# Optimization experiments

Measured on AMD Instinct MI355X. Metric: run time of the kernel, lower is better.

The kernel has to match this reference:

```python
import jax, jax.numpy as jnp
import numpy as np

CLIP_FRAMES = 16
CLIP_STRIDE = 8
D_CODE = 256
K_CODE = 8192
ENC_DIM = 128 * CLIP_FRAMES * 4 * 4  # 32768
EPS = 1e-5


def setup_inputs() -> dict:
    key = jax.random.key(0)
    ks = jax.random.split(key, 16)
    rn = lambda k, s, sc: (jax.random.normal(k, s, jnp.float32) * sc)
    inp = {}
    inp['x'] = jax.random.normal(ks[0], (4, 3, 64, 96, 96), jnp.float32)
    inp['conv1_w'] = rn(ks[1], (32, 3, 3, 3, 3), 0.1)
    inp['conv1_b'] = jnp.zeros((32,), jnp.float32)
    inp['bn1_g'] = jnp.ones((32,), jnp.float32)
    inp['bn1_b'] = jnp.zeros((32,), jnp.float32)
    inp['conv2_w'] = rn(ks[2], (64, 32, 3, 3, 3), 0.05)
    inp['conv2_b'] = jnp.zeros((64,), jnp.float32)
    inp['bn2_g'] = jnp.ones((64,), jnp.float32)
    inp['bn2_b'] = jnp.zeros((64,), jnp.float32)
    inp['conv3_w'] = rn(ks[3], (128, 64, 3, 3, 3), 0.04)
    inp['conv3_b'] = jnp.zeros((128,), jnp.float32)
    inp['bn3_g'] = jnp.ones((128,), jnp.float32)
    inp['bn3_b'] = jnp.zeros((128,), jnp.float32)
    inp['proj_w'] = rn(ks[4], (D_CODE, ENC_DIM), 0.005)
    inp['proj_b'] = jnp.zeros((D_CODE,), jnp.float32)
    inp['codebook'] = jax.random.uniform(ks[5], (K_CODE, D_CODE), jnp.float32, -1.0 / K_CODE, 1.0 / K_CODE)
    inp['gru_w_ih'] = rn(ks[6], (3 * D_CODE, D_CODE), 0.05)
    inp['gru_w_hh'] = rn(ks[7], (3 * D_CODE, D_CODE), 0.05)
    inp['gru_b_ih'] = jnp.zeros((3 * D_CODE,), jnp.float32)
    inp['gru_b_hh'] = jnp.zeros((3 * D_CODE,), jnp.float32)
    return inp


def _conv3d(x, w, b):
    y = jax.lax.conv_general_dilated(x, w, (1, 1, 1), ((1, 1), (1, 1), (1, 1)),
                                     dimension_numbers=('NCDHW', 'OIDHW', 'NCDHW'))
    return y + b[None, :, None, None, None]


def _bn(x, g, b):
    # training-mode BatchNorm3d: batch stats over (N,D,H,W), biased variance
    m = x.mean(axis=(0, 2, 3, 4), keepdims=True)
    v = ((x - m) ** 2).mean(axis=(0, 2, 3, 4), keepdims=True)
    return g[None, :, None, None, None] * (x - m) * jax.lax.rsqrt(v + EPS) + b[None, :, None, None, None]


def _maxpool(x):
    return jax.lax.reduce_window(x, -jnp.inf, jax.lax.max, (1, 1, 1, 2, 2), (1, 1, 1, 2, 2), 'VALID')


def _adaptive_avgpool(x):
    # [N,128,16,24,24] -> [N,128,16,4,4]; 24/4=6 exact window
    s = jax.lax.reduce_window(x, 0.0, jax.lax.add, (1, 1, 1, 6, 6), (1, 1, 1, 6, 6), 'VALID')
    return s / 36.0


def _gru(xs, w_ih, w_hh, b_ih, b_hh):
    # torch GRU, batch_first, h0=0. xs: [B,L,D]
    B, L, D = xs.shape
    gx = jnp.einsum('bld,gd->blg', xs, w_ih) + b_ih  # [B,L,3D]

    def step(h, gx_t):
        gh = h @ w_hh.T + b_hh
        xr, xz, xn = jnp.split(gx_t, 3, axis=-1)
        hr, hz, hn = jnp.split(gh, 3, axis=-1)
        r = jax.nn.sigmoid(xr + hr)
        z = jax.nn.sigmoid(xz + hz)
        n = jnp.tanh(xn + r * hn)
        h2 = (1.0 - z) * n + z * h
        return h2, h2

    h0 = jnp.zeros((B, D), xs.dtype)
    _, ys = jax.lax.scan(step, h0, jnp.swapaxes(gx, 0, 1))
    return jnp.swapaxes(ys, 0, 1)  # [B,L,D]


def _forward(x, conv1_w, conv1_b, bn1_g, bn1_b, conv2_w, conv2_b, bn2_g, bn2_b,
             conv3_w, conv3_b, bn3_g, bn3_b, proj_w, proj_b, codebook,
             gru_w_ih, gru_w_hh, gru_b_ih, gru_b_hh):
    B, C, T, H, W = x.shape
    num_clips = max(1, (T - CLIP_FRAMES) // CLIP_STRIDE + 1)
    clips = jnp.stack([x[:, :, i * CLIP_STRIDE:i * CLIP_STRIDE + CLIP_FRAMES] for i in range(num_clips)])

    def encode(clip):  # clip: [B,3,16,96,96]; BN stats per-clip like the torch loop
        h = jax.nn.relu(_bn(_conv3d(clip, conv1_w, conv1_b), bn1_g, bn1_b))
        h = _maxpool(h)
        h = jax.nn.relu(_bn(_conv3d(h, conv2_w, conv2_b), bn2_g, bn2_b))
        h = _maxpool(h)
        h = jax.nn.relu(_bn(_conv3d(h, conv3_w, conv3_b), bn3_g, bn3_b))
        h = _adaptive_avgpool(h)            # [B,128,16,4,4]
        h = h.reshape(B, -1)                # [B, 32768]
        return h @ proj_w.T + proj_b        # [B, D_CODE]

    features = jnp.swapaxes(jax.vmap(encode)(clips), 0, 1)  # [B,L,D]
    L, D = features.shape[1], features.shape[2]

    # quantize: squared-Euclidean argmin (same argmin as torch.cdist p=2)
    flat = features.reshape(-1, D)
    d2 = (flat * flat).sum(-1, keepdims=True) - 2.0 * flat @ codebook.T + (codebook * codebook).sum(-1)
    token_indices = jnp.argmin(d2, axis=-1)
    quantized = codebook[token_indices].reshape(B, L, D)

    sg = jax.lax.stop_gradient
    commitment_loss = jnp.mean((features - sg(quantized)) ** 2)
    codebook_loss = jnp.mean((quantized - sg(features)) ** 2)
    context_features = _gru(quantized[:, :-1], gru_w_ih, gru_w_hh, gru_b_ih, gru_b_hh)
    context_loss = jnp.mean((context_features - features[:, 1:]) ** 2)
    vq_loss = commitment_loss + 0.25 * codebook_loss + 0.1 * context_loss
    return token_indices.reshape(B, L), quantized, commitment_loss, codebook_loss, context_loss, vq_loss


def reference(x, conv1_w, conv1_b, bn1_g, bn1_b, conv2_w, conv2_b, bn2_g, bn2_b,
              conv3_w, conv3_b, bn3_g, bn3_b, proj_w, proj_b, codebook,
              gru_w_ih, gru_w_hh, gru_b_ih, gru_b_hh):
    return _forward(x, conv1_w, conv1_b, bn1_g, bn1_b, conv2_w, conv2_b, bn2_g, bn2_b,
                    conv3_w, conv3_b, bn3_g, bn3_b, proj_w, proj_b, codebook,
                    gru_w_ih, gru_w_hh, gru_b_ih, gru_b_hh)
```

## Files before the change

### kernel.cpp

```cpp
#include <hip/hip_runtime.h>
#include <math.h>


typedef __attribute__((ext_vector_type(8))) short short8;
typedef __attribute__((ext_vector_type(4))) float f32x4;

__device__ inline unsigned short f2bf(float x) {
    unsigned int u = __float_as_uint(x);
    u += 0x7FFFu + ((u >> 16) & 1u);
    return (unsigned short)(u >> 16);
}
__device__ inline float bf2f(unsigned short h) {
    return __uint_as_float(((unsigned int)h) << 16);
}
__device__ inline f32x4 vmax4(f32x4 a, f32x4 b) {
    return (f32x4){fmaxf(a.x, b.x), fmaxf(a.y, b.y), fmaxf(a.z, b.z), fmaxf(a.w, b.w)};
}
__device__ inline f32x4 vmin4(f32x4 a, f32x4 b) {
    return (f32x4){fminf(a.x, b.x), fminf(a.y, b.y), fminf(a.z, b.z), fminf(a.w, b.w)};
}

#define C1LOADR(J) \
    f32x4 u = *(const f32x4*)(ip + (J) * 36); \
    f32x4 w4 = *(const f32x4*)(ip + (J) * 36 + 4); \
    f32x4 sA = u; \
    f32x4 sB = __builtin_shufflevector(u, w4, 1, 2, 3, 4); \
    f32x4 sC = __builtin_shufflevector(u, w4, 2, 3, 4, 5);
#define C1UPD0(I) a0_##I += wa0 * sA + wa1 * sB + wa2 * sC; a1_##I += wb0 * sA + wb1 * sB + wb2 * sC;
#define C1UPD1(I) a0_##I += wa3 * sA + wa4 * sB + wa5 * sC; a1_##I += wb3 * sA + wb4 * sB + wb5 * sC;
#define C1UPD2(I) a0_##I += wa6 * sA + wa7 * sB + wa8 * sC; a1_##I += wb6 * sA + wb7 * sB + wb8 * sC;

__launch_bounds__(256, 3)
__global__ void conv1k(const float* __restrict__ x, const float* __restrict__ wgt,
                       const float* __restrict__ bias, float* __restrict__ pmax,
                       float* __restrict__ pmin, float* __restrict__ stats, int t0) {
    int bb = blockIdx.x;
    int xt = bb % 3; int yt = (bb / 3) % 4; int t = (bb / 12) % 16; int n = bb / 192;
    int x0 = xt * 32, y0 = yt * 24;
    __shared__ float tile[9 * 936];
    __shared__ float wl[3456];
    __shared__ float sst[64];
    int tid = threadIdx.x;
    for (int i = tid; i < 3456; i += 256) {
        int idx = i % 12; int r = i / 12;
        int co = r & 31; int p = r >> 5;
        wl[i] = idx < 9 ? wgt[co * 81 + p * 9 + idx] : 0.f;
    }
    if (tid < 64) sst[tid] = 0.f;
    for (int i = tid; i < 7956; i += 256) {
        int p = i / 884; int rem = i % 884;
        int r = rem / 34, cl = rem % 34;
        int ci = p / 3, kt = p % 3;
        int lt = t + kt - 1;
        int yy = y0 + r - 1, xx = x0 + cl - 1;
        float v = 0.f;
        if (lt >= 0 && lt <= 15 && yy >= 0 && yy < 96 && xx >= 0 && xx < 96)
            v = x[((size_t)(n * 3 + ci) * 64 + (t0 + lt)) * 9216 + yy * 96 + cl + x0 - 1];
        tile[p * 936 + r * 36 + cl] = v;
    }
    __syncthreads();

    int cg = tid & 15;
    int co0 = cg * 2;
    float bv0 = bias[co0], bv1 = bias[co0 + 1];
    float ls0 = 0.f, lq0 = 0.f, ls1 = 0.f, lq1 = 0.f;
    size_t nt48 = (size_t)(n * 16 + t) * 48;

    #pragma unroll 1
    for (int rr = 0; rr < 3; ++rr) {
        int sp = rr * 16 + (tid >> 4);
        int tx = sp & 7, ty = sp >> 3;
        f32x4 a0_0 = (f32x4)bv0, a0_1 = (f32x4)bv0, a0_2 = (f32x4)bv0, a0_3 = (f32x4)bv0;
        f32x4 a1_0 = (f32x4)bv1, a1_1 = (f32x4)bv1, a1_2 = (f32x4)bv1, a1_3 = (f32x4)bv1;

        #pragma unroll 1
        for (int p = 0; p < 9; ++p) {
            const float* wpk = wl + ((p * 32 + co0) * 12);
            f32x4 wv0 = *(const f32x4*)(wpk);
            f32x4 wv1 = *(const f32x4*)(wpk + 4);
            f32x4 wv2 = *(const f32x4*)(wpk + 8);
            f32x4 wv3 = *(const f32x4*)(wpk + 12);
            f32x4 wv4 = *(const f32x4*)(wpk + 16);
            f32x4 wv5 = *(const f32x4*)(wpk + 20);
            float wa0 = wv0.x, wa1 = wv0.y, wa2 = wv0.z, wa3 = wv0.w;
            float wa4 = wv1.x, wa5 = wv1.y, wa6 = wv1.z, wa7 = wv1.w;
            float wa8 = wv2.x;
            float wb0 = wv3.x, wb1 = wv3.y, wb2 = wv3.z, wb3 = wv3.w;
            float wb4 = wv4.x, wb5 = wv4.y, wb6 = wv4.z, wb7 = wv4.w;
            float wb8 = wv5.x;
            const float* ip = tile + p * 936 + (ty * 4) * 36 + tx * 4;
            { C1LOADR(0) C1UPD0(0) }
            { C1LOADR(1) C1UPD0(1) C1UPD1(0) }
            { C1LOADR(2) C1UPD0(2) C1UPD1(1) C1UPD2(0) }
            { C1LOADR(3) C1UPD0(3) C1UPD1(2) C1UPD2(1) }
            { C1LOADR(4) C1UPD1(3) C1UPD2(2) }
            { C1LOADR(5) C1UPD2(3) }
        }

        f32x4 s4 = a0_0 + a0_1 + a0_2 + a0_3;
        ls0 += s4.x + s4.y + s4.z + s4.w;
        f32x4 q4 = a0_0 * a0_0 + a0_1 * a0_1 + a0_2 * a0_2 + a0_3 * a0_3;
        lq0 += q4.x + q4.y + q4.z + q4.w;
        f32x4 s5 = a1_0 + a1_1 + a1_2 + a1_3;
        ls1 += s5.x + s5.y + s5.z + s5.w;
        f32x4 q5 = a1_0 * a1_0 + a1_1 * a1_1 + a1_2 * a1_2 + a1_3 * a1_3;
        lq1 += q5.x + q5.y + q5.z + q5.w;

        f32x4 mx0a = vmax4(a0_0, a0_1), mx0b = vmax4(a0_2, a0_3);
        f32x4 mn0a = vmin4(a0_0, a0_1), mn0b = vmin4(a0_2, a0_3);
        f32x4 mx1a = vmax4(a1_0, a1_1), mx1b = vmax4(a1_2, a1_3);
        f32x4 mn1a = vmin4(a1_0, a1_1), mn1b = vmin4(a1_2, a1_3);
        size_t row0 = (nt48 + (size_t)(yt * 12 + ty * 2)) * 1536 + (size_t)(xt * 16 + tx * 2) * 32 + co0;
        size_t row1 = row0 + 1536;
        *(float2*)(pmax + row0)      = make_float2(fmaxf(mx0a.x, mx0a.y), fmaxf(mx1a.x, mx1a.y));
        *(float2*)(pmax + row0 + 32) = make_float2(fmaxf(mx0a.z, mx0a.w), fmaxf(mx1a.z, mx1a.w));
        *(float2*)(pmax + row1)      = make_float2(fmaxf(mx0b.x, mx0b.y), fmaxf(mx1b.x, mx1b.y));
        *(float2*)(pmax + row1 + 32) = make_float2(fmaxf(mx0b.z, mx0b.w), fmaxf(mx1b.z, mx1b.w));
        *(float2*)(pmin + row0)      = make_float2(fminf(mn0a.x, mn0a.y), fminf(mn1a.x, mn1a.y));
        *(float2*)(pmin + row0 + 32) = make_float2(fminf(mn0a.z, mn0a.w), fminf(mn1a.z, mn1a.w));
        *(float2*)(pmin + row1)      = make_float2(fminf(mn0b.x, mn0b.y), fminf(mn1b.x, mn1b.y));
        *(float2*)(pmin + row1 + 32) = make_float2(fminf(mn0b.z, mn0b.w), fminf(mn1b.z, mn1b.w));
    }

    ls0 += __shfl_xor(ls0, 16, 64); ls0 += __shfl_xor(ls0, 32, 64);
    lq0 += __shfl_xor(lq0, 16, 64); lq0 += __shfl_xor(lq0, 32, 64);
    ls1 += __shfl_xor(ls1, 16, 64); ls1 += __shfl_xor(ls1, 32, 64);
    lq1 += __shfl_xor(lq1, 16, 64); lq1 += __shfl_xor(lq1, 32, 64);
    if ((tid & 63) < 16) {
        atomicAdd(&sst[co0 * 2], ls0);
        atomicAdd(&sst[co0 * 2 + 1], lq0);
        atomicAdd(&sst[co0 * 2 + 2], ls1);
        atomicAdd(&sst[co0 * 2 + 3], lq1);
    }
    __syncthreads();
    if (tid < 64) atomicAdd(&stats[tid], sst[tid]);
}

__global__ void bnpool1b(const float* __restrict__ pmax, const float* __restrict__ pmin,
                         const float* __restrict__ st, const float* __restrict__ gam,
                         const float* __restrict__ bet,
                         unsigned short* __restrict__ phi, unsigned short* __restrict__ plo) {
    int i = blockIdx.x * 256 + threadIdx.x;
    int c8 = i & 3; int xo = (i >> 2) % 48; int yo = (i / 192) % 48;
    int t = (i / 9216) % 16; int n = i / 147456;
    size_t base = (((size_t)(n * 16 + t) * 48 + yo) * 48 + xo) * 32 + c8 * 8;
    union { unsigned short s[8]; uint4 v; } Uh, Ul;
    #pragma unroll
    for (int j = 0; j < 8; ++j) {
        int ch = c8 * 8 + j;
        float mean = st[ch * 2] * (1.f / 589824.f);
        float var  = st[ch * 2 + 1] * (1.f / 589824.f) - mean * mean;
        var = var < 0.f ? 0.f : var;
        float sc = gam[ch] / sqrtf(var + 1e-5f);
        float sh = bet[ch] - mean * sc;
        float pv = sc >= 0.f ? pmax[base + j] : pmin[base + j];
        float v = fmaxf(sc * pv + sh, 0.f);
        Uh.s[j] = f2bf(v);
        Ul.s[j] = f2bf(v - bf2f(Uh.s[j]));
    }
    size_t off = ((((size_t)n * 18 + t + 1) * 50 + yo + 1) * 52 + (xo + 1)) * 32 + c8 * 8;
    *(uint4*)(phi + off) = Uh.v;
    *(uint4*)(plo + off) = Ul.v;
}

__launch_bounds__(256, 2)
__global__ void conv2k(const unsigned short* __restrict__ phi, const unsigned short* __restrict__ plo,
                       const unsigned short* __restrict__ w2p, const float* __restrict__ bias,
                       float* __restrict__ out, float* __restrict__ st) {
    __shared__ unsigned short lds[36864];
    __shared__ float sred[4][64], qred[4][64];
    int b = blockIdx.x;
    int y0 = (b % 12) * 4; int t = (b / 12) % 16; int n = b / 192;
    int wv = threadIdx.x >> 6, lane = threadIdx.x & 63;
    int c = lane & 15, q = lane >> 4;
    int y = y0 + wv;

    f32x4 acc[4][3];
    #pragma unroll
    for (int i = 0; i < 4; ++i)
        #pragma unroll
        for (int j = 0; j < 3; ++j) acc[i][j] = (f32x4)0.f;

    const int laneoff = c * 32 + q * 8;
    for (int kt = 0; kt < 3; ++kt) {
        const uint4* src = (const uint4*)(w2p + kt * 36864);
        uint4* dst = (uint4*)lds;
        __syncthreads();
        for (int i = threadIdx.x; i < 4608; i += 256) dst[i] = src[i];
        __syncthreads();
        const unsigned short* ph_t = phi + ((size_t)(n * 18 + t + kt) * 50) * (52 * 32);
        const unsigned short* pl_t = plo + ((size_t)(n * 18 + t + kt) * 50) * (52 * 32);
        #pragma unroll
        for (int ky = 0; ky < 3; ++ky) {
            const unsigned short* rowh = ph_t + (y + ky) * (52 * 32) + laneoff;
            const unsigned short* rowl = pl_t + (y + ky) * (52 * 32) + laneoff;
            #pragma unroll
            for (int kx = 0; kx < 3; ++kx) {
                int o = ky * 3 + kx;
                const unsigned short* wb = lds + o * 4096 + laneoff;
                short8 ah[4], al[4], bh[3], bl[3];
                #pragma unroll
                for (int mb = 0; mb < 4; ++mb) {
                    ah[mb] = *(const short8*)(wb + mb * 512);
                    al[mb] = *(const short8*)(wb + 2048 + mb * 512);
                }
                #pragma unroll
                for (int xt = 0; xt < 3; ++xt) {
                    bh[xt] = *(const short8*)(rowh + (xt * 16 + kx) * 32);
                    bl[xt] = *(const short8*)(rowl + (xt * 16 + kx) * 32);
                }
                #pragma unroll
                for (int mb = 0; mb < 4; ++mb)
                    #pragma unroll
                    for (int xt = 0; xt < 3; ++xt) {
                        acc[mb][xt] = __builtin_amdgcn_mfma_f32_16x16x32_bf16(ah[mb], bh[xt], acc[mb][xt], 0, 0, 0);
                        acc[mb][xt] = __builtin_amdgcn_mfma_f32_16x16x32_bf16(ah[mb], bl[xt], acc[mb][xt], 0, 0, 0);
                        acc[mb][xt] = __builtin_amdgcn_mfma_f32_16x16x32_bf16(al[mb], bh[xt], acc[mb][xt], 0, 0, 0);
                    }
            }
        }
    }
    float* ob = out + (((size_t)(n * 16 + t) * 48) + y) * (48 * 64);
    #pragma unroll
    for (int mb = 0; mb < 4; ++mb) {
        f32x4 bv = *(const f32x4*)(bias + mb * 16 + q * 4);
        f32x4 v0 = acc[mb][0] + bv, v1 = acc[mb][1] + bv, v2 = acc[mb][2] + bv;
        *(f32x4*)(ob + (0 * 16 + c) * 64 + mb * 16 + q * 4) = v0;
        *(f32x4*)(ob + (1 * 16 + c) * 64 + mb * 16 + q * 4) = v1;
        *(f32x4*)(ob + (2 * 16 + c) * 64 + mb * 16 + q * 4) = v2;
        #pragma unroll
        for (int r = 0; r < 4; ++r) {
            float s  = v0[r] + v1[r] + v2[r];
            float q2 = v0[r] * v0[r] + v1[r] * v1[r] + v2[r] * v2[r];
            #pragma unroll
            for (int m = 1; m < 16; m <<= 1) { s += __shfl_xor(s, m, 64); q2 += __shfl_xor(q2, m, 64); }
            if (c == 0) { sred[wv][mb * 16 + q * 4 + r] = s; qred[wv][mb * 16 + q * 4 + r] = q2; }
        }
    }
    __syncthreads();
    if (threadIdx.x < 64) {
        float s = sred[0][threadIdx.x] + sred[1][threadIdx.x] + sred[2][threadIdx.x] + sred[3][threadIdx.x];
        float q2 = qred[0][threadIdx.x] + qred[1][threadIdx.x] + qred[2][threadIdx.x] + qred[3][threadIdx.x];
        atomicAdd(&st[threadIdx.x * 2], s);
        atomicAdd(&st[threadIdx.x * 2 + 1], q2);
    }
}

__global__ void bnpool2k(const float* __restrict__ cin, const float* __restrict__ st,
                         const float* __restrict__ gam, const float* __restrict__ bet,
                         unsigned short* __restrict__ phi, unsigned short* __restrict__ plo) {
    int i = blockIdx.x * 256 + threadIdx.x;
    if (i >= 509184) return;
    int oc = i & 7; int xp = (i >> 3) % 34; int yp = (i / 272) % 26;
    int tp = (i / 7072) % 18; int n = i / 127296;
    union { unsigned short s[8]; uint4 v; } Uh, Ul;
    if (tp >= 1 && tp <= 16 && yp >= 1 && yp <= 24 && xp >= 1 && xp <= 24) {
        int t = tp - 1, yo = yp - 1, xo = xp - 1;
        const float* b0 = cin + ((((size_t)(n * 16 + t) * 48) + 2 * yo) * 48 + 2 * xo) * 64 + oc * 8;
        #pragma unroll
        for (int j = 0; j < 8; ++j) {
            int ch = oc * 8 + j;
            float mean = st[ch * 2] * (1.f / 147456.f);
            float var  = st[ch * 2 + 1] * (1.f / 147456.f) - mean * mean;
            var = var < 0.f ? 0.f : var;
            float sc = gam[ch] / sqrtf(var + 1e-5f);
            float sh = bet[ch] - mean * sc;
            float a  = b0[j] * sc + sh;
            float bb = b0[64 + j] * sc + sh;
            float c2 = b0[3072 + j] * sc + sh;
            float d  = b0[3136 + j] * sc + sh;
            float v = fmaxf(fmaxf(fmaxf(a, bb), fmaxf(c2, d)), 0.f);
            Uh.s[j] = f2bf(v);
            Ul.s[j] = f2bf(v - bf2f(Uh.s[j]));
        }
    } else {
        Uh.v = make_uint4(0, 0, 0, 0);
        Ul.v = make_uint4(0, 0, 0, 0);
    }
    size_t off = ((((size_t)n * 18 + tp) * 26 + yp) * 34 + xp) * 64 + oc * 8;
    *(uint4*)(phi + off) = Uh.v;
    *(uint4*)(plo + off) = Ul.v;
}

__launch_bounds__(256, 3)
__global__ void conv3k(const unsigned short* __restrict__ phi, const unsigned short* __restrict__ plo,
                       const unsigned short* __restrict__ w3p, const float* __restrict__ bias,
                       float* __restrict__ out, float* __restrict__ st) {
    __shared__ unsigned short lds[24576];
    __shared__ float sred[4][64], qred[4][64];
    int b = blockIdx.x;
    int y0 = (b % 6) * 4; int t = (b / 6) % 16; int n = (b / 96) % 4; int cg = b / 384;
    int wv = threadIdx.x >> 6, lane = threadIdx.x & 63;
    int c = lane & 15, q = lane >> 4;
    int y = y0 + wv;

    f32x4 acc[4][2];
    #pragma unroll
    for (int i = 0; i < 4; ++i) { acc[i][0] = (f32x4)0.f; acc[i][1] = (f32x4)0.f; }

    const int laneoff = c * 64 + q * 8;
    const int aoff = c * 32 + q * 8;
    const unsigned short* wsrc = w3p + (size_t)cg * 221184;

    for (int kt = 0; kt < 3; ++kt) {
        const unsigned short* ph_t = phi + (size_t)(n * 18 + t + kt) * (26 * 34 * 64);
        const unsigned short* pl_t = plo + (size_t)(n * 18 + t + kt) * (26 * 34 * 64);
        for (int ky = 0; ky < 3; ++ky) {
            const uint4* src = (const uint4*)(wsrc + (kt * 3 + ky) * 24576);
            uint4* dst = (uint4*)lds;
            __syncthreads();
            for (int i = threadIdx.x; i < 3072; i += 256) dst[i] = src[i];
            __syncthreads();
            const unsigned short* rowh = ph_t + (y + ky) * (34 * 64) + laneoff;
            const unsigned short* rowl = pl_t + (y + ky) * (34 * 64) + laneoff;
            #pragma unroll
            for (int kx = 0; kx < 3; ++kx) {
                #pragma unroll
                for (int kc = 0; kc < 2; ++kc) {
                    const unsigned short* wb = lds + kx * 8192 + kc * 2048 + aoff;
                    short8 ah[4], al[4], bh[2], bl[2];
                    #pragma unroll
                    for (int mb = 0; mb < 4; ++mb) {
                        ah[mb] = *(const short8*)(wb + mb * 512);
                        al[mb] = *(const short8*)(wb + 4096 + mb * 512);
                    }
                    #pragma unroll
                    for (int xt = 0; xt < 2; ++xt) {
                        bh[xt] = *(const short8*)(rowh + (xt * 16 + kx) * 64 + kc * 32);
                        bl[xt] = *(const short8*)(rowl + (xt * 16 + kx) * 64 + kc * 32);
                    }
                    #pragma unroll
                    for (int mb = 0; mb < 4; ++mb)
                        #pragma unroll
                        for (int xt = 0; xt < 2; ++xt) {
                            acc[mb][xt] = __builtin_amdgcn_mfma_f32_16x16x32_bf16(ah[mb], bh[xt], acc[mb][xt], 0, 0, 0);
                            acc[mb][xt] = __builtin_amdgcn_mfma_f32_16x16x32_bf16(ah[mb], bl[xt], acc[mb][xt], 0, 0, 0);
                            acc[mb][xt] = __builtin_amdgcn_mfma_f32_16x16x32_bf16(al[mb], bh[xt], acc[mb][xt], 0, 0, 0);
                        }
                }
            }
        }
    }
    float* ob = out + (((size_t)(n * 16 + t) * 24) + y) * (24 * 128) + cg * 64;
    #pragma unroll
    for (int mb = 0; mb < 4; ++mb) {
        f32x4 bv = *(const f32x4*)(bias + cg * 64 + mb * 16 + q * 4);
        f32x4 v0 = acc[mb][0] + bv;
        f32x4 v1 = acc[mb][1] + bv;
        *(f32x4*)(ob + c * 128 + mb * 16 + q * 4) = v0;
        if (c < 8) *(f32x4*)(ob + (16 + c) * 128 + mb * 16 + q * 4) = v1;
        #pragma unroll
        for (int r = 0; r < 4; ++r) {
            float s  = v0[r] + (c < 8 ? v1[r] : 0.f);
            float q2 = v0[r] * v0[r] + (c < 8 ? v1[r] * v1[r] : 0.f);
            #pragma unroll
            for (int m = 1; m < 16; m <<= 1) { s += __shfl_xor(s, m, 64); q2 += __shfl_xor(q2, m, 64); }
            if (c == 0) { sred[wv][mb * 16 + q * 4 + r] = s; qred[wv][mb * 16 + q * 4 + r] = q2; }
        }
    }
    __syncthreads();
    if (threadIdx.x < 64) {
        int co = cg * 64 + threadIdx.x;
        float s = sred[0][threadIdx.x] + sred[1][threadIdx.x] + sred[2][threadIdx.x] + sred[3][threadIdx.x];
        float q2 = qred[0][threadIdx.x] + qred[1][threadIdx.x] + qred[2][threadIdx.x] + qred[3][threadIdx.x];
        atomicAdd(&st[co * 2], s);
        atomicAdd(&st[co * 2 + 1], q2);
    }
}

__global__ void bnavgk(const float* __restrict__ x, const float* __restrict__ st,
                       const float* __restrict__ gam, const float* __restrict__ bet,
                       float* __restrict__ enc) {
    int i = blockIdx.x * 256 + threadIdx.x;
    int c = i & 127; int xo = (i >> 7) & 3; int yo = (i >> 9) & 3;
    int t = (i >> 11) & 15; int n = i >> 15;
    float mean = st[c * 2] * (1.f / 36864.f);
    float var  = st[c * 2 + 1] * (1.f / 36864.f) - mean * mean;
    var = var < 0.f ? 0.f : var;
    float sc = gam[c] / sqrtf(var + 1e-5f);
    float sh = bet[c] - mean * sc;
    const float* base = x + ((((size_t)(n * 16 + t) * 24) + yo * 6) * 24 + xo * 6) * 128 + c;
    float s = 0.f;
    #pragma unroll
    for (int wy = 0; wy < 6; ++wy)
        #pragma unroll
        for (int wx = 0; wx < 6; ++wx)
            s += fmaxf(base[(wy * 24 + wx) * 128] * sc + sh, 0.f);
    enc[(size_t)n * 32768 + (size_t)c * 256 + t * 16 + yo * 4 + xo] = s * (1.f / 36.f);
}

__global__ void prep2k(const float* __restrict__ c2w, unsigned short* __restrict__ w2p) {
    int i = blockIdx.x * 256 + threadIdx.x;
    if (i >= 110592) return;
    int ci = i & 31; int co = (i >> 5) & 63; int h = (i >> 11) & 1;
    int o = (i >> 12) % 9; int kt = i / 36864;
    int ky = o / 3, kx = o % 3;
    float w = c2w[(((size_t)(co * 32 + ci) * 3 + kt) * 3 + ky) * 3 + kx];
    unsigned short hi = f2bf(w);
    w2p[i] = h ? f2bf(w - bf2f(hi)) : hi;
}
__global__ void prep3k(const float* __restrict__ c3w, unsigned short* __restrict__ w3p) {
    int i = blockIdx.x * 256 + threadIdx.x;
    if (i >= 442368) return;
    int cil = i & 31; int cop = (i >> 5) & 63; int kc = (i >> 11) & 1; int h = (i >> 12) & 1;
    int kx = (i >> 13) % 3; int ky = (i / 24576) % 3; int kt = (i / 73728) % 3; int cg = i / 221184;
    int ci = kc * 32 + cil; int co = cg * 64 + cop;
    float w = c3w[(((size_t)(co * 64 + ci) * 3 + kt) * 3 + ky) * 3 + kx];
    unsigned short hi = f2bf(w);
    w3p[i] = h ? f2bf(w - bf2f(hi)) : hi;
}
__global__ void prepwhhk(const float* __restrict__ whh, float* __restrict__ wt) {
    int i = blockIdx.x * 256 + threadIdx.x;
    int g = i % 768, k = i / 768;
    wt[i] = whh[(size_t)g * 256 + k];
}

__global__ void transck(const float* __restrict__ cb, float* __restrict__ cbT) {
    __shared__ float t[32][33];
    int bx = blockIdx.x & 255;
    int by = blockIdx.x >> 8;
    int ld = threadIdx.x & 31, lk = threadIdx.x >> 5;
    #pragma unroll
    for (int i = 0; i < 4; ++i) {
        int kl = lk + i * 8;
        t[kl][ld] = cb[(size_t)(bx * 32 + kl) * 256 + by * 32 + ld];
    }
    __syncthreads();
    #pragma unroll
    for (int i = 0; i < 4; ++i) {
        int dl = lk + i * 8;
        cbT[(size_t)(by * 32 + dl) * 8192 + bx * 32 + ld] = t[ld][dl];
    }
}

__global__ void cnormk(const float* __restrict__ cbT, double* __restrict__ cn2) {
    int k = blockIdx.x * 256 + threadIdx.x;
    double s = 0.0;
    for (int d = 0; d < 256; ++d) {
        double c = (double)cbT[(size_t)d * 8192 + k];
        s += c * c;
    }
    cn2[k] = s;
}

__global__ void projinitk(const float* __restrict__ pb, float* __restrict__ feat) {
    int i = blockIdx.x * 256 + threadIdx.x;
    feat[i] = pb[i & 255];
}

__global__ void projk(const float* __restrict__ enc, const float* __restrict__ pw,
                      float* __restrict__ feat) {
    int d = blockIdx.x & 255; int ch = blockIdx.x >> 8;
    int k0 = ch * 4096;
    float acc[28];
    #pragma unroll
    for (int e = 0; e < 28; ++e) acc[e] = 0.f;
    const float* wrow = pw + (size_t)d * 32768 + k0;
    for (int k = threadIdx.x; k < 4096; k += 256) {
        float wv = wrow[k];
        #pragma unroll
        for (int e = 0; e < 28; ++e) acc[e] += enc[(size_t)e * 32768 + k0 + k] * wv;
    }
    __shared__ float red[4 * 28];
    #pragma unroll
    for (int e = 0; e < 28; ++e) {
        float v = acc[e];
        #pragma unroll
        for (int o = 32; o > 0; o >>= 1) v += __shfl_down(v, o, 64);
        if ((threadIdx.x & 63) == 0) red[(threadIdx.x >> 6) * 28 + e] = v;
    }
    __syncthreads();
    if (threadIdx.x < 28) {
        int e = threadIdx.x;
        int l = e >> 2, n = e & 3;
        float s = red[e] + red[28 + e] + red[56 + e] + red[84 + e];
        atomicAdd(&feat[(size_t)(n * 7 + l) * 256 + d], s);
    }
}

__global__ void quantk(const float* __restrict__ feat, const float* __restrict__ cbT,
                       const double* __restrict__ cn2, unsigned long long* __restrict__ best) {
    int kc = blockIdx.x & 31, r = blockIdx.x >> 5;
    int k = kc * 256 + threadIdx.x;
    __shared__ float fs[256];
    fs[threadIdx.x] = feat[(size_t)r * 256 + threadIdx.x];
    __syncthreads();
    double dot = 0.0;
    for (int d = 0; d < 256; ++d)
        dot += (double)cbT[(size_t)d * 8192 + k] * (double)fs[d];
    float s = (float)(cn2[k] - 2.0 * dot);
    unsigned int bits = __float_as_uint(s);
    unsigned int key = (bits & 0x80000000u) ? ~bits : (bits | 0x80000000u);
    unsigned long long p = ((unsigned long long)key << 32) | (unsigned int)k;
    #pragma unroll
    for (int o = 32; o > 0; o >>= 1) {
        unsigned long long qv = __shfl_down(p, o, 64);
        if (qv < p) p = qv;
    }
    if ((threadIdx.x & 63) == 0) atomicMin(&best[r], p);
}

__global__ void gatherk(const unsigned long long* __restrict__ best,
                        const float* __restrict__ feat, const float* __restrict__ cb,
                        float* __restrict__ dout, float* __restrict__ quant,
                        float* __restrict__ acc) {
    int r = blockIdx.x;
    int d = threadIdx.x;
    int idx = (int)(best[r] & 0xFFFFFFFFull);
    float q = cb[(size_t)idx * 256 + d];
    quant[r * 256 + d] = q;
    dout[28 + r * 256 + d] = q;
    if (d == 0) dout[r] = (float)idx;
    float df = feat[r * 256 + d] - q;
    float v = df * df;
    #pragma unroll
    for (int o = 32; o > 0; o >>= 1) v += __shfl_down(v, o, 64);
    if ((d & 63) == 0) atomicAdd(&acc[0], v);
}

__global__ void gxk(const float* __restrict__ quant, const float* __restrict__ wih,
                    const float* __restrict__ bih, float* __restrict__ gx) {
    int o = blockIdx.x * 256 + threadIdx.x;
    int g = o % 768; int t = (o / 768) % 6; int n = o / (768 * 6);
    const float* q = quant + (size_t)(n * 7 + t) * 256;
    const float* w = wih + (size_t)g * 256;
    float s = bih[g];
    #pragma unroll 4
    for (int d = 0; d < 256; ++d) s += q[d] * w[d];
    gx[o] = s;
}

__global__ void gru_allk(const float* __restrict__ gx, const float* __restrict__ wt,
                         const float* __restrict__ bhh, const float* __restrict__ feat,
                         float* __restrict__ acc) {
    int b = blockIdx.x;
    int d = threadIdx.x;
    __shared__ float hs[256];
    hs[d] = 0.f;
    __syncthreads();
    float ctx = 0.f;
    for (int t = 0; t < 6; ++t) {
        float g0 = bhh[d], g1 = bhh[256 + d], g2 = bhh[512 + d];
        #pragma unroll 4
        for (int k = 0; k < 256; ++k) {
            float hv = hs[k];
            const float* wr = wt + (size_t)k * 768;
            g0 += wr[d] * hv; g1 += wr[256 + d] * hv; g2 += wr[512 + d] * hv;
        }
        const float* gxr = gx + (size_t)(b * 6 + t) * 768;
        float xr = gxr[d], xz = gxr[256 + d], xn = gxr[512 + d];
        float rr = 1.f / (1.f + expf(-(xr + g0)));
        float zz = 1.f / (1.f + expf(-(xz + g1)));
        float nn = tanhf(xn + rr * g2);
        float h2 = (1.f - zz) * nn + zz * hs[d];
        __syncthreads();
        hs[d] = h2;
        __syncthreads();
        float df = h2 - feat[(size_t)(b * 7 + t + 1) * 256 + d];
        ctx += df * df;
    }
    #pragma unroll
    for (int o = 32; o > 0; o >>= 1) ctx += __shfl_down(ctx, o, 64);
    if ((d & 63) == 0) atomicAdd(&acc[1], ctx);
}

__global__ void fink(const float* __restrict__ acc, float* __restrict__ dout) {
    float comm = acc[0] / 7168.f;
    float ctx  = acc[1] / 6144.f;
    dout[7196] = comm;
    dout[7197] = comm;
    dout[7198] = ctx;
    dout[7199] = comm + 0.25f * comm + 0.1f * ctx;
}

extern "C" void kernel_launch(void* const* d_in, const int* in_sizes, int n_in,
                              void* d_out, int out_size, void* d_ws, size_t ws_size,
                              hipStream_t stream) {
    (void)in_sizes; (void)n_in; (void)out_size; (void)ws_size;
    const float* x    = (const float*)d_in[0];
    const float* c1w  = (const float*)d_in[1];
    const float* c1b  = (const float*)d_in[2];
    const float* bn1g = (const float*)d_in[3];
    const float* bn1b = (const float*)d_in[4];
    const float* c2w  = (const float*)d_in[5];
    const float* c2b  = (const float*)d_in[6];
    const float* bn2g = (const float*)d_in[7];
    const float* bn2b = (const float*)d_in[8];
    const float* c3w  = (const float*)d_in[9];
    const float* c3b  = (const float*)d_in[10];
    const float* bn3g = (const float*)d_in[11];
    const float* bn3b = (const float*)d_in[12];
    const float* pw   = (const float*)d_in[13];
    const float* pb   = (const float*)d_in[14];
    const float* cb   = (const float*)d_in[15];
    const float* wih  = (const float*)d_in[16];
    const float* whh  = (const float*)d_in[17];
    const float* bih  = (const float*)d_in[18];
    const float* bhh  = (const float*)d_in[19];
    float* out = (float*)d_out;

    char* w = (char*)d_ws;
    float* A  = (float*)w;                         w += 75497472;
    float* PMAX = A;
    float* PMIN = A + 4718592;
    float* cbT = A;
    double* cn2 = (double*)((char*)A + 8388608);
    char*  SH = w;                                 w += 16293888;
    unsigned short* P3h = (unsigned short*)SH;
    unsigned short* P3l = (unsigned short*)(SH + 8146944);
    unsigned short* P2h = (unsigned short*)w;      w += 11980800;
    unsigned short* P2l = (unsigned short*)w;      w += 11980800;
    unsigned short* W2P = (unsigned short*)w;      w += 221184;
    unsigned short* W3P = (unsigned short*)w;      w += 884736;
    float* WT    = (float*)w;                      w += 786432;
    float* enc   = (float*)w;                      w += 3670016;
    float* feat  = (float*)w;                      w += 28672;
    float* quant = (float*)w;                      w += 28672;
    float* gx    = (float*)w;                      w += 73728;
    float* statsA = (float*)w;                     w += 21504;
    float* acc    = (float*)w;                     w += 16;
    unsigned long long* best = (unsigned long long*)w;  w += 224;

    hipMemsetAsync(P2h, 0, 11980800 * 2, stream);
    hipMemsetAsync(statsA, 0, 21504 + 16, stream);
    hipMemsetAsync(best, 0xFF, 224, stream);
    prep2k<<<432, 256, 0, stream>>>(c2w, W2P);
    prep3k<<<1728, 256, 0, stream>>>(c3w, W3P);
    prepwhhk<<<768, 256, 0, stream>>>(whh, WT);

    for (int l = 0; l < 7; ++l) {
        float* st1 = statsA + (l * 3 + 0) * 256;
        float* st2 = statsA + (l * 3 + 1) * 256;
        float* st3 = statsA + (l * 3 + 2) * 256;
        conv1k<<<768, 256, 0, stream>>>(x, c1w, c1b, PMAX, PMIN, st1, l * 8);
        bnpool1b<<<2304, 256, 0, stream>>>(PMAX, PMIN, st1, bn1g, bn1b, P2h, P2l);
        conv2k<<<768, 256, 0, stream>>>(P2h, P2l, W2P, c2b, A, st2);
        bnpool2k<<<1989, 256, 0, stream>>>(A, st2, bn2g, bn2b, P3h, P3l);
        conv3k<<<768, 256, 0, stream>>>(P3h, P3l, W3P, c3b, A, st3);
        bnavgk<<<512, 256, 0, stream>>>(A, st3, bn3g, bn3b, enc + (size_t)l * 131072);
    }

    transck<<<2048, 256, 0, stream>>>(cb, cbT);
    cnormk<<<32, 256, 0, stream>>>(cbT, cn2);
    projinitk<<<28, 256, 0, stream>>>(pb, feat);
    projk<<<2048, 256, 0, stream>>>(enc, pw, feat);
    quantk<<<896, 256, 0, stream>>>(feat, cbT, cn2, best);
    gatherk<<<28, 256, 0, stream>>>(best, feat, cb, out, quant, acc);
    gxk<<<72, 256, 0, stream>>>(quant, wih, bih, gx);
    gru_allk<<<4, 256, 0, stream>>>(gx, WT, bhh, feat, acc);
    fink<<<1, 1, 0, stream>>>(acc, out);
}
```

Measured before the change: 2.411 ms.

## Stage input tiles in LDS and stream weights from global in conv2/conv3

Conv2 and conv3 previously staged weight slices in shared memory and read the activation rows straight from global memory. Both kernels now stage the hi/lo bf16 input tile (6 rows by full width, per temporal tap) in shared memory and load the weight fragments directly from global/L2. Conv3 XOR-swizzles the channel groups in shared memory to avoid bank conflicts. This shrinks the LDS footprint, allowing conv2's launch bound to rise to 3 blocks per CU, and halves conv3's barrier count by staging once per temporal tap instead of per ky. The cost is weight fragment loads from L2 inside the MFMA inner loop, plus `#pragma unroll 1` on ky, which may expose memory latency.

```diff
diff --git a/kernel.cpp b/kernel.cpp
--- a/kernel.cpp
+++ b/kernel.cpp
@@ -163,11 +163,11 @@
     *(uint4*)(plo + off) = Ul.v;
 }
 
-__launch_bounds__(256, 2)
+__launch_bounds__(256, 3)
 __global__ void conv2k(const unsigned short* __restrict__ phi, const unsigned short* __restrict__ plo,
                        const unsigned short* __restrict__ w2p, const float* __restrict__ bias,
                        float* __restrict__ out, float* __restrict__ st) {
-    __shared__ unsigned short lds[36864];
+    __shared__ unsigned short tin[2 * 6 * 52 * 32];
     __shared__ float sred[4][64], qred[4][64];
     int b = blockIdx.x;
     int y0 = (b % 12) * 4; int t = (b / 12) % 16; int n = b / 192;
@@ -181,23 +181,24 @@
         #pragma unroll
         for (int j = 0; j < 3; ++j) acc[i][j] = (f32x4)0.f;
 
-    const int laneoff = c * 32 + q * 8;
     for (int kt = 0; kt < 3; ++kt) {
-        const uint4* src = (const uint4*)(w2p + kt * 36864);
-        uint4* dst = (uint4*)lds;
+        const unsigned short* srch = phi + (size_t)(n * 18 + t + kt) * (50 * 52 * 32);
+        const unsigned short* srcl = plo + (size_t)(n * 18 + t + kt) * (50 * 52 * 32);
         __syncthreads();
-        for (int i = threadIdx.x; i < 4608; i += 256) dst[i] = src[i];
+        for (int i = threadIdx.x; i < 2496; i += 256) {
+            int g = i & 3; int xx = (i >> 2) % 52; int rh = (i >> 2) / 52;
+            int row = rh % 6; int h = rh / 6;
+            const unsigned short* src = (h ? srcl : srch) + (size_t)(y0 + row) * 1664 + xx * 32 + g * 8;
+            *(uint4*)(tin + ((rh * 52 + xx) << 5) + (g << 3)) = *(const uint4*)src;
+        }
         __syncthreads();
-        const unsigned short* ph_t = phi + ((size_t)(n * 18 + t + kt) * 50) * (52 * 32);
-        const unsigned short* pl_t = plo + ((size_t)(n * 18 + t + kt) * 50) * (52 * 32);
-        #pragma unroll
+        const unsigned short* wkt = w2p + kt * 36864 + c * 32 + q * 8;
+        #pragma unroll 1
         for (int ky = 0; ky < 3; ++ky) {
-            const unsigned short* rowh = ph_t + (y + ky) * (52 * 32) + laneoff;
-            const unsigned short* rowl = pl_t + (y + ky) * (52 * 32) + laneoff;
+            int row = wv + ky;
             #pragma unroll
             for (int kx = 0; kx < 3; ++kx) {
-                int o = ky * 3 + kx;
-                const unsigned short* wb = lds + o * 4096 + laneoff;
+                const unsigned short* wb = wkt + (ky * 3 + kx) * 4096;
                 short8 ah[4], al[4], bh[3], bl[3];
                 #pragma unroll
                 for (int mb = 0; mb < 4; ++mb) {
@@ -206,8 +207,9 @@
                 }
                 #pragma unroll
                 for (int xt = 0; xt < 3; ++xt) {
-                    bh[xt] = *(const short8*)(rowh + (xt * 16 + kx) * 32);
-                    bl[xt] = *(const short8*)(rowl + (xt * 16 + kx) * 32);
+                    int xx = xt * 16 + kx + c;
+                    bh[xt] = *(const short8*)(tin + ((row * 52 + xx) << 5) + (q << 3));
+                    bl[xt] = *(const short8*)(tin + (((6 + row) * 52 + xx) << 5) + (q << 3));
                 }
                 #pragma unroll
                 for (int mb = 0; mb < 4; ++mb)
@@ -286,7 +288,7 @@
 __global__ void conv3k(const unsigned short* __restrict__ phi, const unsigned short* __restrict__ plo,
                        const unsigned short* __restrict__ w3p, const float* __restrict__ bias,
                        float* __restrict__ out, float* __restrict__ st) {
-    __shared__ unsigned short lds[24576];
+    __shared__ unsigned short tin[2 * 6 * 34 * 64];
     __shared__ float sred[4][64], qred[4][64];
     int b = blockIdx.x;
     int y0 = (b % 6) * 4; int t = (b / 6) % 16; int n = (b / 96) % 4; int cg = b / 384;
@@ -298,26 +300,29 @@
     #pragma unroll
     for (int i = 0; i < 4; ++i) { acc[i][0] = (f32x4)0.f; acc[i][1] = (f32x4)0.f; }
 
-    const int laneoff = c * 64 + q * 8;
-    const int aoff = c * 32 + q * 8;
-    const unsigned short* wsrc = w3p + (size_t)cg * 221184;
+    const unsigned short* wsrc = w3p + (size_t)cg * 221184 + c * 32 + q * 8;
 
     for (int kt = 0; kt < 3; ++kt) {
-        const unsigned short* ph_t = phi + (size_t)(n * 18 + t + kt) * (26 * 34 * 64);
-        const unsigned short* pl_t = plo + (size_t)(n * 18 + t + kt) * (26 * 34 * 64);
+        const unsigned short* srch = phi + (size_t)(n * 18 + t + kt) * (26 * 34 * 64);
+        const unsigned short* srcl = plo + (size_t)(n * 18 + t + kt) * (26 * 34 * 64);
+        __syncthreads();
+        for (int i = threadIdx.x; i < 3264; i += 256) {
+            int g = i & 7; int xx = (i >> 3) % 34; int rh = (i >> 3) / 34;
+            int row = rh % 6; int h = rh / 6;
+            const unsigned short* src = (h ? srcl : srch) + (size_t)(y0 + row) * 2176 + xx * 64 + g * 8;
+            *(uint4*)(tin + ((rh * 34 + xx) << 6) + ((g ^ (xx & 7)) << 3)) = *(const uint4*)src;
+        }
+        __syncthreads();
+        const unsigned short* wkt = wsrc + kt * 73728;
+        #pragma unroll 1
         for (int ky = 0; ky < 3; ++ky) {
-            const uint4* src = (const uint4*)(wsrc + (kt * 3 + ky) * 24576);
-            uint4* dst = (uint4*)lds;
-            __syncthreads();
-            for (int i = threadIdx.x; i < 3072; i += 256) dst[i] = src[i];
-            __syncthreads();
-            const unsigned short* rowh = ph_t + (y + ky) * (34 * 64) + laneoff;
-            const unsigned short* rowl = pl_t + (y + ky) * (34 * 64) + laneoff;
+            int row = wv + ky;
+            const unsigned short* wky = wkt + ky * 24576;
             #pragma unroll
             for (int kx = 0; kx < 3; ++kx) {
                 #pragma unroll
                 for (int kc = 0; kc < 2; ++kc) {
-                    const unsigned short* wb = lds + kx * 8192 + kc * 2048 + aoff;
+                    const unsigned short* wb = wky + kx * 8192 + kc * 2048;
                     short8 ah[4], al[4], bh[2], bl[2];
                     #pragma unroll
                     for (int mb = 0; mb < 4; ++mb) {
@@ -326,8 +331,10 @@
                     }
                     #pragma unroll
                     for (int xt = 0; xt < 2; ++xt) {
-                        bh[xt] = *(const short8*)(rowh + (xt * 16 + kx) * 64 + kc * 32);
-                        bl[xt] = *(const short8*)(rowl + (xt * 16 + kx) * 64 + kc * 32);
+                        int xx = xt * 16 + kx + c;
+                        int so = ((kc * 4 + q) ^ (xx & 7)) << 3;
+                        bh[xt] = *(const short8*)(tin + ((row * 34 + xx) << 6) + so);
+                        bl[xt] = *(const short8*)(tin + (((6 + row) * 34 + xx) << 6) + so);
                     }
                     #pragma unroll
                     for (int mb = 0; mb < 4; ++mb)
```

After: 2.699 ms. +11.9%, slower.
